# Performance work log

Hardware: AMD Instinct MI355X
Metric: run time of the kernel (lower is better)

Reference implementation:

```python
import jax, jax.numpy as jnp
import numpy as np

ALPHA = 0.2  # LeakyReLU negative slope
NEG_INF = -9e15


def setup_inputs() -> dict:
    key = jax.random.key(0)
    k1, k2, k3, k4 = jax.random.split(key, 4)
    N, F_IN, F_OUT = 8192, 128, 64
    h = jax.random.normal(k1, (N, F_IN), dtype=jnp.float32)
    adj = jax.random.randint(k2, (N, N), 0, 2, dtype=jnp.int32)
    # xavier_uniform with gain=1.414 (as in the torch module)
    gain = 1.414
    bW = gain * np.sqrt(6.0 / (F_IN + F_OUT))
    W = jax.random.uniform(k3, (F_IN, F_OUT), dtype=jnp.float32, minval=-bW, maxval=bW)
    ba = gain * np.sqrt(6.0 / (2 * F_OUT + 1))
    a = jax.random.uniform(k4, (2 * F_OUT, 1), dtype=jnp.float32, minval=-ba, maxval=ba)
    return {"h": h, "adj": adj, "W": W, "a": a}


def reference(h, adj, W, a):
    # Wh: [N, F_out]
    Wh = h @ W
    F_out = Wh.shape[1]
    # Decompose a^T [Wh_i || Wh_j] = (Wh @ a_src)_i + (Wh @ a_dst)_j
    # (same math as the repeat+concat construction, without the N*N*2F tensor)
    src = Wh @ a[:F_out, 0]   # [N]
    dst = Wh @ a[F_out:, 0]   # [N]
    e = jax.nn.leaky_relu(src[:, None] + dst[None, :], negative_slope=ALPHA)  # [N, N]
    e = jnp.where(adj > 0, e, jnp.float32(NEG_INF))
    attention = jax.nn.softmax(e, axis=1)  # [N, N]
    h_prime = attention @ Wh               # [N, F_out]
    return jax.nn.elu(h_prime)
```

## Files before the change

### kernel.cpp

```cpp
#include <hip/hip_runtime.h>

#define ALPHA 0.2f
#define NN 8192
#define FIN 128
#define FOUT 64

typedef short bf16x8 __attribute__((ext_vector_type(8)));
typedef float f32x4 __attribute__((ext_vector_type(4)));

__device__ __forceinline__ unsigned short f2b(float x) {
    unsigned u = __builtin_bit_cast(unsigned, x);
    unsigned r = (u + 0x7fffu + ((u >> 16) & 1u)) >> 16;
    return (unsigned short)r;
}

__global__ __launch_bounds__(256) void gat_k1(const float* __restrict__ h,
                                              const float* __restrict__ W,
                                              const float* __restrict__ a,
                                              float* __restrict__ Wh,
                                              float* __restrict__ src,
                                              float* __restrict__ dst) {
    __shared__ float wlds[FIN * FOUT];
    int t = threadIdx.x;
    const float4* W4 = (const float4*)W;
    float4* wlds4 = (float4*)wlds;
#pragma unroll
    for (int q = 0; q < 8; ++q) wlds4[q * 256 + t] = W4[q * 256 + t];
    __syncthreads();
    int wave = t >> 6, lane = t & 63;
    int row = blockIdx.x * 4 + wave;
    const float4* h4 = (const float4*)(h + (size_t)row * FIN);
    float acc = 0.f;
#pragma unroll
    for (int k4 = 0; k4 < 32; ++k4) {
        float4 hv = h4[k4];
        acc = fmaf(hv.x, wlds[(k4 * 4 + 0) * 64 + lane], acc);
        acc = fmaf(hv.y, wlds[(k4 * 4 + 1) * 64 + lane], acc);
        acc = fmaf(hv.z, wlds[(k4 * 4 + 2) * 64 + lane], acc);
        acc = fmaf(hv.w, wlds[(k4 * 4 + 3) * 64 + lane], acc);
    }
    Wh[(size_t)row * 64 + lane] = acc;
    float sa = acc * a[lane];
    float da = acc * a[64 + lane];
#pragma unroll
    for (int off = 32; off; off >>= 1) {
        sa += __shfl_xor(sa, off);
        da += __shfl_xor(da, off);
    }
    if (lane == 0) { src[row] = sa; dst[row] = da; }
}

__global__ __launch_bounds__(256) void gat_k1b(const float* __restrict__ Wh,
                                               unsigned short* __restrict__ whbt) {
    __shared__ unsigned short t16[64 * 68];
    int t = threadIdx.x;
    int rb = blockIdx.x * 64;
    const float4* s4 = (const float4*)(Wh + (size_t)rb * 64);
#pragma unroll
    for (int q = 0; q < 4; ++q) {
        float4 v = s4[t * 4 + q];
        int flat = t * 16 + q * 4;
        int r = flat >> 6, f = flat & 63;
        unsigned short* p = &t16[r * 68 + f];
        p[0] = f2b(v.x); p[1] = f2b(v.y); p[2] = f2b(v.z); p[3] = f2b(v.w);
    }
    __syncthreads();
    int f = t >> 2, qr = t & 3;
    unsigned v[8];
#pragma unroll
    for (int k = 0; k < 8; ++k) {
        unsigned lo = t16[(qr * 16 + 2 * k + 0) * 68 + f];
        unsigned hi = t16[(qr * 16 + 2 * k + 1) * 68 + f];
        v[k] = lo | (hi << 16);
    }
    uint4* o = (uint4*)(whbt + (size_t)f * NN + rb + qr * 16);
    o[0] = make_uint4(v[0], v[1], v[2], v[3]);
    o[1] = make_uint4(v[4], v[5], v[6], v[7]);
}

__global__ __launch_bounds__(256) void gat_k2(const int* __restrict__ adj,
                                              const unsigned short* __restrict__ whbt,
                                              const float* __restrict__ src,
                                              const float* __restrict__ dst,
                                              float* __restrict__ pl,
                                              float* __restrict__ pacc,
                                              int ns, int js) {
    const int l = threadIdx.x & 63;
    const int w = threadIdx.x >> 6;
    const int r = l & 15;
    const int g = l >> 4;
    const int s = blockIdx.x;
    const int rg = blockIdx.y;
    const int task = rg * ns + s;
    const int row = rg * 64 + w * 16 + r;
    const int j0 = s * js, jend = j0 + js;

    const float srcv = src[row];
    const int4* adjr = (const int4*)(adj + (size_t)row * NN);
    const float4* dst4 = (const float4*)dst;

    f32x4 acc0 = {0.f, 0.f, 0.f, 0.f}, acc1 = acc0, acc2 = acc0, acc3 = acc0, accl = acc0;
    bf16x8 bones;
#pragma unroll
    for (int e = 0; e < 8; ++e) bones[e] = (short)0x3F80;

    int base = (j0 >> 2) + 2 * g;
    int4 c0 = adjr[base], c1 = adjr[base + 1], c2 = adjr[base + 8], c3 = adjr[base + 9];

    for (int jc = j0; jc < jend; jc += 64) {
        int nj = jc + 64;
        int pj = (nj < jend) ? nj : j0;
        int nb = (pj >> 2) + 2 * g;
        int4 n0 = adjr[nb], n1 = adjr[nb + 1], n2 = adjr[nb + 8], n3 = adjr[nb + 9];

#pragma unroll
        for (int half = 0; half < 2; ++half) {
            const int jh = jc + half * 32;
            int4 ca = half ? c2 : c0;
            int4 cb = half ? c3 : c1;
            float4 d0 = dst4[(jh >> 2) + 2 * g];
            float4 d1 = dst4[(jh >> 2) + 2 * g + 1];
            float xs[8] = {d0.x, d0.y, d0.z, d0.w, d1.x, d1.y, d1.z, d1.w};
            int ms[8] = {ca.x, ca.y, ca.z, ca.w, cb.x, cb.y, cb.z, cb.w};
            float p[8];
#pragma unroll
            for (int e = 0; e < 8; ++e) {
                float x = srcv + xs[e];
                float lr = fmaxf(x, 0.f) + ALPHA * fminf(x, 0.f);
                float pe = __expf(lr);
                p[e] = (ms[e] != 0) ? pe : 0.f;
            }
            unsigned pw0, pw1, pw2, pw3;
            asm("v_cvt_pk_bf16_f32 %0, %1, %2" : "=v"(pw0) : "v"(p[0]), "v"(p[1]));
            asm("v_cvt_pk_bf16_f32 %0, %1, %2" : "=v"(pw1) : "v"(p[2]), "v"(p[3]));
            asm("v_cvt_pk_bf16_f32 %0, %1, %2" : "=v"(pw2) : "v"(p[4]), "v"(p[5]));
            asm("v_cvt_pk_bf16_f32 %0, %1, %2" : "=v"(pw3) : "v"(p[6]), "v"(p[7]));
            uint4 pwv = make_uint4(pw0, pw1, pw2, pw3);
            bf16x8 af = __builtin_bit_cast(bf16x8, pwv);

            const unsigned short* bbase = whbt + (size_t)r * NN + jh + 8 * g;
            bf16x8 b0 = *(const bf16x8*)(bbase + 0 * 16 * NN);
            bf16x8 b1 = *(const bf16x8*)(bbase + 1 * 16 * NN);
            bf16x8 b2 = *(const bf16x8*)(bbase + 2 * 16 * NN);
            bf16x8 b3 = *(const bf16x8*)(bbase + 3 * 16 * NN);
            acc0 = __builtin_amdgcn_mfma_f32_16x16x32_bf16(af, b0, acc0, 0, 0, 0);
            acc1 = __builtin_amdgcn_mfma_f32_16x16x32_bf16(af, b1, acc1, 0, 0, 0);
            acc2 = __builtin_amdgcn_mfma_f32_16x16x32_bf16(af, b2, acc2, 0, 0, 0);
            acc3 = __builtin_amdgcn_mfma_f32_16x16x32_bf16(af, b3, acc3, 0, 0, 0);
            accl = __builtin_amdgcn_mfma_f32_16x16x32_bf16(af, bones, accl, 0, 0, 0);
        }
        c0 = n0; c1 = n1; c2 = n2; c3 = n3;
    }

    if (r == 0) {
        float* plo = pl + (size_t)task * 64 + w * 16 + g * 4;
        plo[0] = accl[0]; plo[1] = accl[1]; plo[2] = accl[2]; plo[3] = accl[3];
    }

    float* po = pacc + (size_t)task * 4096 + (size_t)(w * 16) * 64;
#pragma unroll
    for (int reg = 0; reg < 4; ++reg) {
        int m = g * 4 + reg;
        po[m * 64 + 0 * 16 + r] = acc0[reg];
        po[m * 64 + 1 * 16 + r] = acc1[reg];
        po[m * 64 + 2 * 16 + r] = acc2[reg];
        po[m * 64 + 3 * 16 + r] = acc3[reg];
    }
}

__global__ __launch_bounds__(256) void gat_k3(const float* __restrict__ pl,
                                              const float* __restrict__ pacc,
                                              float* __restrict__ out, int ns) {
    int t = threadIdx.x;
    int wave = t >> 6, lane = t & 63;
    int row = blockIdx.x * 4 + wave;
    int rg = row >> 6, rr = row & 63;
    float L = 0.f, o = 0.f;
    for (int s2 = 0; s2 < ns; ++s2) {
        L += pl[(size_t)(rg * ns + s2) * 64 + rr];
        o += pacc[(size_t)(rg * ns + s2) * 4096 + rr * 64 + lane];
    }
    float hp = o / L;
    out[(size_t)row * 64 + lane] = hp > 0.f ? hp : __expf(hp) - 1.f;
}

extern "C" void kernel_launch(void* const* d_in, const int* in_sizes, int n_in,
                              void* d_out, int out_size, void* d_ws, size_t ws_size,
                              hipStream_t stream) {
    const float* h = (const float*)d_in[0];
    const int* adj = (const int*)d_in[1];
    const float* W = (const float*)d_in[2];
    const float* a = (const float*)d_in[3];
    float* out = (float*)d_out;
    float* ws = (float*)d_ws;

    size_t avail = ws_size / sizeof(float);
    int ns = 8;
    while (ns > 1 && (size_t)802816 + (size_t)ns * 532480 > avail) ns >>= 1;
    int js = NN / ns;

    float* Wh = ws;
    float* src = Wh + (size_t)NN * FOUT;
    float* dst = src + NN;
    float* pl = dst + NN;
    float* pacc = pl + (size_t)128 * ns * 64;
    unsigned short* whbt = (unsigned short*)(pacc + (size_t)128 * ns * 4096);

    gat_k1<<<dim3(NN / 4), dim3(256), 0, stream>>>(h, W, a, Wh, src, dst);
    gat_k1b<<<dim3(NN / 64), dim3(256), 0, stream>>>(Wh, whbt);
    gat_k2<<<dim3(ns, 128), dim3(256), 0, stream>>>(adj, whbt, src, dst, pl, pacc, ns, js);
    gat_k3<<<dim3(NN / 4), dim3(256), 0, stream>>>(pl, pacc, out, ns);
}
```

Baseline: 426.1 us.

## Pack adjacency into bitmasks in a prepass and read bits in attention kernel

Adds a prepass kernel that reads the int32 adjacency matrix once and ballots it into 64-bit masks, one bit per edge. The attention kernel then loads these compact masks instead of int4 adjacency words. The split count drops from 8 to 4 to fit the extra workspace. The full 256 MB adjacency read still happens, now in the prepass, so the gain hinges on the main kernel being latency-bound rather than bandwidth-bound. The change adds a launch and a bitmask write, and runs the main kernel with fewer blocks.

```diff
diff --git a/kernel.cpp b/kernel.cpp
--- a/kernel.cpp
+++ b/kernel.cpp
@@ -12,6 +12,27 @@
     unsigned u = __builtin_bit_cast(unsigned, x);
     unsigned r = (u + 0x7fffu + ((u >> 16) & 1u)) >> 16;
     return (unsigned short)r;
+}
+
+__global__ __launch_bounds__(256) void gat_k0(const int* __restrict__ adj,
+                                              unsigned long long* __restrict__ adjb) {
+    int t = threadIdx.x, w = t >> 6, l = t & 63;
+    int row = blockIdx.x * 4 + w;
+    const int4* a4 = (const int4*)(adj + (size_t)row * NN);
+    unsigned long long* ob = adjb + (size_t)row * 32 * 4;
+#pragma unroll 4
+    for (int it = 0; it < 32; ++it) {
+        int4 av = a4[it * 64 + l];
+        unsigned long long b0 = __ballot(av.x != 0);
+        unsigned long long b1 = __ballot(av.y != 0);
+        unsigned long long b2 = __ballot(av.z != 0);
+        unsigned long long b3 = __ballot(av.w != 0);
+        if (l == 0) {
+            ulonglong4 v;
+            v.x = b0; v.y = b1; v.z = b2; v.w = b3;
+            *(ulonglong4*)(ob + it * 4) = v;
+        }
+    }
 }
 
 __global__ __launch_bounds__(256) void gat_k1(const float* __restrict__ h,
@@ -78,7 +99,7 @@
     o[1] = make_uint4(v[4], v[5], v[6], v[7]);
 }
 
-__global__ __launch_bounds__(256) void gat_k2(const int* __restrict__ adj,
+__global__ __launch_bounds__(256) void gat_k2(const unsigned long long* __restrict__ adjb,
                                               const unsigned short* __restrict__ whbt,
                                               const float* __restrict__ src,
                                               const float* __restrict__ dst,
@@ -93,42 +114,44 @@
     const int rg = blockIdx.y;
     const int task = rg * ns + s;
     const int row = rg * 64 + w * 16 + r;
-    const int j0 = s * js, jend = j0 + js;
+    const int j0 = s * js;
 
     const float srcv = src[row];
-    const int4* adjr = (const int4*)(adj + (size_t)row * NN);
     const float4* dst4 = (const float4*)dst;
+    const unsigned long long* brow = adjb + (size_t)row * 32 * 4;
 
     f32x4 acc0 = {0.f, 0.f, 0.f, 0.f}, acc1 = acc0, acc2 = acc0, acc3 = acc0, accl = acc0;
     bf16x8 bones;
 #pragma unroll
     for (int e = 0; e < 8; ++e) bones[e] = (short)0x3F80;
 
-    int base = (j0 >> 2) + 2 * g;
-    int4 c0 = adjr[base], c1 = adjr[base + 1], c2 = adjr[base + 8], c3 = adjr[base + 9];
-
-    for (int jc = j0; jc < jend; jc += 64) {
-        int nj = jc + 64;
-        int pj = (nj < jend) ? nj : j0;
-        int nb = (pj >> 2) + 2 * g;
-        int4 n0 = adjr[nb], n1 = adjr[nb + 1], n2 = adjr[nb + 8], n3 = adjr[nb + 9];
-
-#pragma unroll
-        for (int half = 0; half < 2; ++half) {
-            const int jh = jc + half * 32;
-            int4 ca = half ? c2 : c0;
-            int4 cb = half ? c3 : c1;
+    const int g0 = j0 >> 8, g1 = (j0 + js) >> 8;
+    ulonglong2 mA = *(const ulonglong2*)(brow + g0 * 4);
+    ulonglong2 mB = *(const ulonglong2*)(brow + g0 * 4 + 2);
+
+    for (int grp = g0; grp < g1; ++grp) {
+        int ng = (grp + 1 < g1) ? grp + 1 : g0;
+        ulonglong2 nA = *(const ulonglong2*)(brow + ng * 4);
+        ulonglong2 nB = *(const ulonglong2*)(brow + ng * 4 + 2);
+        unsigned long long m0 = mA.x, m1 = mA.y, m2 = mB.x, m3 = mB.y;
+        const int jgrp = grp << 8;
+#pragma unroll 2
+        for (int hh = 0; hh < 8; ++hh) {
+            const int jh = jgrp + hh * 32;
+            const int hb = hh * 8 + 2 * g;
             float4 d0 = dst4[(jh >> 2) + 2 * g];
             float4 d1 = dst4[(jh >> 2) + 2 * g + 1];
             float xs[8] = {d0.x, d0.y, d0.z, d0.w, d1.x, d1.y, d1.z, d1.w};
-            int ms[8] = {ca.x, ca.y, ca.z, ca.w, cb.x, cb.y, cb.z, cb.w};
             float p[8];
 #pragma unroll
             for (int e = 0; e < 8; ++e) {
                 float x = srcv + xs[e];
                 float lr = fmaxf(x, 0.f) + ALPHA * fminf(x, 0.f);
                 float pe = __expf(lr);
-                p[e] = (ms[e] != 0) ? pe : 0.f;
+                unsigned long long mm = (e & 3) == 0 ? m0 : (e & 3) == 1 ? m1
+                                      : (e & 3) == 2 ? m2 : m3;
+                unsigned bit = (unsigned)(mm >> (hb + (e >> 2))) & 1u;
+                p[e] = bit ? pe : 0.f;
             }
             unsigned pw0, pw1, pw2, pw3;
             asm("v_cvt_pk_bf16_f32 %0, %1, %2" : "=v"(pw0) : "v"(p[0]), "v"(p[1]));
@@ -149,7 +172,7 @@
             acc3 = __builtin_amdgcn_mfma_f32_16x16x32_bf16(af, b3, acc3, 0, 0, 0);
             accl = __builtin_amdgcn_mfma_f32_16x16x32_bf16(af, bones, accl, 0, 0, 0);
         }
-        c0 = n0; c1 = n1; c2 = n2; c3 = n3;
+        mA = nA; mB = nB;
     }
 
     if (r == 0) {
@@ -195,8 +218,8 @@
     float* ws = (float*)d_ws;
 
     size_t avail = ws_size / sizeof(float);
-    int ns = 8;
-    while (ns > 1 && (size_t)802816 + (size_t)ns * 532480 > avail) ns >>= 1;
+    int ns = 4;
+    while (ns > 1 && (size_t)2899968 + (size_t)ns * 532480 > avail) ns >>= 1;
     int js = NN / ns;
 
     float* Wh = ws;
@@ -205,9 +228,11 @@
     float* pl = dst + NN;
     float* pacc = pl + (size_t)128 * ns * 64;
     unsigned short* whbt = (unsigned short*)(pacc + (size_t)128 * ns * 4096);
-
+    unsigned long long* adjb = (unsigned long long*)((float*)whbt + 262144);
+
+    gat_k0<<<dim3(NN / 4), dim3(256), 0, stream>>>(adj, adjb);
     gat_k1<<<dim3(NN / 4), dim3(256), 0, stream>>>(h, W, a, Wh, src, dst);
     gat_k1b<<<dim3(NN / 64), dim3(256), 0, stream>>>(Wh, whbt);
-    gat_k2<<<dim3(ns, 128), dim3(256), 0, stream>>>(adj, whbt, src, dst, pl, pacc, ns, js);
+    gat_k2<<<dim3(ns, 128), dim3(256), 0, stream>>>(adjb, whbt, src, dst, pl, pacc, ns, js);
     gat_k3<<<dim3(NN / 4), dim3(256), 0, stream>>>(pl, pacc, out, ns);
 }
```

Result: slower. 455.2 us (+6.8%).
